# Kernel optimization log

Measured on AMD Instinct MI355X. Metric: run time of the kernel, lower is better.

Reference implementation:

```python
import jax, jax.numpy as jnp
import numpy as np

NUM_PT = 13
NUM_SQ = 64
SQPT = NUM_SQ * NUM_PT            # 832
NUM_FEATURES = NUM_SQ * SQPT      # 53248
ATTN_TABLE = NUM_SQ * SQPT * SQPT # 44302336
DEPTH = 256
DFF = 1024
NUM_HEADS = 4
N = 512
LN_EPS = 1e-5


def layer_norm(x, w, b):
    m = jnp.mean(x, axis=-1, keepdims=True)
    v = jnp.mean(jnp.square(x - m), axis=-1, keepdims=True)
    return (x - m) * jax.lax.rsqrt(v + LN_EPS) * w + b


def setup_inputs() -> dict:
    key = jax.random.key(0)
    ks = jax.random.split(key, 12)
    # indices must satisfy piece_indices = ksq*832 + offset, offset in [0,832)
    pno = jax.random.randint(ks[0], (N, NUM_SQ), 0, SQPT, dtype=jnp.int32)
    ksq = jax.random.randint(ks[1], (N,), 0, NUM_SQ, dtype=jnp.int32)
    piece_indices = ksq[:, None] * SQPT + pno
    attn_bias_indices = jax.random.randint(ks[2], (N, NUM_SQ * NUM_SQ), 0, NUM_PT * NUM_PT, dtype=jnp.int32)
    f32 = jnp.float32
    return {
        "piece_indices": piece_indices,
        "attn_bias_indices": attn_bias_indices,
        "ksq": ksq,
        "value_table": jax.random.normal(ks[3], (NUM_FEATURES, DEPTH), f32) * 0.02,
        "attn_weights_table": jax.random.normal(ks[4], (ATTN_TABLE, NUM_HEADS), f32) * 0.02,
        "attn_bias_table": jax.random.normal(ks[5], (NUM_PT * NUM_PT, NUM_HEADS), f32) * 0.02,
        "attn_scale": jnp.asarray(100.0, f32),
        "W1": jax.random.normal(ks[6], (DEPTH, DFF), f32) * 0.02,
        "b1": jnp.zeros((DFF,), f32),
        "W2": jax.random.normal(ks[7], (DFF, DEPTH), f32) * 0.02,
        "b2": jnp.zeros((DEPTH,), f32),
        "ln1_w": jnp.ones((DEPTH,), f32),
        "ln1_b": jnp.zeros((DEPTH,), f32),
        "ln2_w": jnp.ones((DEPTH,), f32),
        "ln2_b": jnp.zeros((DEPTH,), f32),
    }


def reference(piece_indices, attn_bias_indices, ksq, value_table, attn_weights_table,
              attn_bias_table, attn_scale, W1, b1, W2, b2, ln1_w, ln1_b, ln2_w, ln2_b):
    n = piece_indices.shape[0]
    dh = DEPTH // NUM_HEADS
    pno = piece_indices - ksq[:, None] * SQPT                      # [N,64] in [0,832)
    attn_idx = (pno[:, :, None] * SQPT + pno[:, None, :]
                + ksq[:, None, None] * SQPT * SQPT)                # [N,64,64]
    aw = attn_weights_table[attn_idx]                              # [N,64,64,H]
    abi = attn_bias_indices.reshape(n, NUM_SQ, NUM_SQ).transpose(0, 2, 1)
    ab = attn_bias_table[abi]                                      # [N,64,64,H]
    logits = ((aw + ab) * attn_scale).transpose(0, 3, 1, 2)        # [N,H,64,64]
    attn = jax.nn.softmax(logits, axis=-1)
    values = value_table[piece_indices].reshape(n, NUM_SQ, NUM_HEADS, dh).transpose(0, 2, 1, 3)  # [N,H,64,dh]
    ctx = jnp.einsum('nhqk,nhkd->nhqd', attn, values) + values
    x = layer_norm(ctx.transpose(0, 2, 1, 3).reshape(n, NUM_SQ, DEPTH), ln1_w, ln1_b)
    ffn = jnp.maximum(x @ W1 + b1, 0.0) @ W2 + b2
    return layer_norm(ffn + x, ln2_w, ln2_b)
```

## Files before the change

kernel.cpp:

```cpp
#include <hip/hip_runtime.h>
#include <stdint.h>

typedef unsigned short u16;
typedef __attribute__((ext_vector_type(8))) short bf16x8;
typedef __attribute__((ext_vector_type(4))) float f32x4;

typedef __attribute__((address_space(1))) const unsigned char gas_u8;
typedef __attribute__((address_space(3))) unsigned char las_u8;

__device__ __forceinline__ void gload_lds16(const void* g, void* l) {
  __builtin_amdgcn_global_load_lds((const gas_u8*)g, (las_u8*)l, 16, 0, 0);
}

__device__ __forceinline__ u16 f2bf(float f) {
  uint32_t u = __float_as_uint(f);
  u += 0x7fffu + ((u >> 16) & 1u);
  return (u16)(u >> 16);
}
__device__ __forceinline__ float bf2f(u16 v) {
  return __uint_as_float(((uint32_t)v) << 16);
}

__global__ __launch_bounds__(256, 4)
void transpose_kernel(const float* __restrict__ W1, u16* __restrict__ W1T,
                      const float* __restrict__ W2, u16* __restrict__ W2T) {
  __shared__ u16 tile[64 * 66];
  int b = blockIdx.x;
  const float* src; u16* dst; int R, C, tc, tr;
  if (b < 64) { src = W1; dst = W1T; R = 256; C = 1024; tc = (b & 15) * 64; tr = (b >> 4) * 64; }
  else { b -= 64; src = W2; dst = W2T; R = 1024; C = 256; tc = (b & 3) * 64; tr = (b >> 2) * 64; }
  const int t = threadIdx.x;
  const int c = t & 63, rb = t >> 6;
#pragma unroll
  for (int i = 0; i < 16; ++i) {
    int r = i * 4 + rb;
    tile[r * 66 + c] = f2bf(src[(size_t)(tr + r) * C + tc + c]);
  }
  __syncthreads();
#pragma unroll
  for (int i = 0; i < 16; ++i) {
    int x = i * 4 + rb;
    int y = c;
    dst[(size_t)(tc + x) * R + tr + y] = tile[y * 66 + x];
  }
}

#define SM_BASE 65536
#define OFF_ABT  (SM_BASE + 0)
#define OFF_PNO  (SM_BASE + 2704)
#define OFF_PIDX (SM_BASE + 2960)
#define OFF_REDA (SM_BASE + 3216)
#define OFF_REDB (SM_BASE + 7312)
#define OFF_RED  (SM_BASE + 11408)
#define OFF_HB   (SM_BASE + 0)

__global__ __launch_bounds__(256, 2)
void mega_kernel(const int* __restrict__ piece_indices,
                 const int* __restrict__ abi_idx,
                 const int* __restrict__ ksq,
                 const float* __restrict__ value_table,
                 const float* __restrict__ aw_table,
                 const float* __restrict__ ab_table,
                 const float* __restrict__ scale_p,
                 const float* __restrict__ ln1w, const float* __restrict__ ln1b,
                 const u16* __restrict__ W1T, const u16* __restrict__ W2T,
                 const float* __restrict__ b1, const float* __restrict__ b2,
                 const float* __restrict__ ln2w, const float* __restrict__ ln2b,
                 float* __restrict__ out) {
  __shared__ __align__(16) char SMEM[79872];
  u16* VT = (u16*)(SMEM);
  u16* P  = (u16*)(SMEM + 32768);
  float* abt_s = (float*)(SMEM + OFF_ABT);
  int* pno_s   = (int*)(SMEM + OFF_PNO);
  int* pidx_s  = (int*)(SMEM + OFF_PIDX);
  float* redA  = (float*)(SMEM + OFF_REDA);
  float* redB  = (float*)(SMEM + OFF_REDB);
  float* red   = (float*)(SMEM + OFF_RED);

  const int n = blockIdx.x;
  const int t = threadIdx.x;
  const int h = t >> 6;
  const int lane = t & 63;
  const int ks = ksq[n];

  if (t < 64) {
    int pi = piece_indices[n * 64 + t];
    pidx_s[t] = pi;
    pno_s[t] = pi - ks * 832;
  }
  for (int i = t; i < 676; i += 256) abt_s[i] = ab_table[i];
  __syncthreads();

  const float scale = scale_p[0];
  const int q = lane, kg = h;

  float l[4][16];
  {
    const int base = ks * (832 * 832) + pno_s[q] * 832;
#pragma unroll
    for (int j = 0; j < 16; ++j) {
      int k = kg * 16 + j;
      int idx = base + pno_s[k];
      f32x4 aw4 = *(const f32x4*)(aw_table + (size_t)idx * 4);
      int bi = abi_idx[n * 4096 + k * 64 + q];
      f32x4 ab4 = *(const f32x4*)(abt_s + bi * 4);
#pragma unroll
      for (int hh = 0; hh < 4; ++hh) l[hh][j] = (aw4[hh] + ab4[hh]) * scale;
    }
  }

  {
    const int feat = t;
#pragma unroll
    for (int c = 0; c < 8; ++c) {
      bf16x8 vv;
#pragma unroll
      for (int j = 0; j < 8; ++j) {
        int k = c * 8 + j;
        float v = value_table[(size_t)pidx_s[k] * 256 + feat];
        vv[j] = (short)f2bf(v);
      }
      int off = feat * 64 + ((c ^ (feat & 7)) << 3);
      *(bf16x8*)(&VT[off]) = vv;
    }
  }

#pragma unroll
  for (int hh = 0; hh < 4; ++hh) {
    float m = l[hh][0];
#pragma unroll
    for (int j = 1; j < 16; ++j) m = fmaxf(m, l[hh][j]);
    redA[(kg * 4 + hh) * 64 + q] = m;
  }
  __syncthreads();
  float inv[4];
#pragma unroll
  for (int hh = 0; hh < 4; ++hh) {
    float m = fmaxf(fmaxf(redA[(0 * 4 + hh) * 64 + q], redA[(1 * 4 + hh) * 64 + q]),
                    fmaxf(redA[(2 * 4 + hh) * 64 + q], redA[(3 * 4 + hh) * 64 + q]));
    float s = 0.f;
#pragma unroll
    for (int j = 0; j < 16; ++j) { l[hh][j] = __expf(l[hh][j] - m); s += l[hh][j]; }
    redB[(kg * 4 + hh) * 64 + q] = s;
  }
  __syncthreads();
#pragma unroll
  for (int hh = 0; hh < 4; ++hh)
    inv[hh] = 1.f / (redB[(0 * 4 + hh) * 64 + q] + redB[(1 * 4 + hh) * 64 + q] +
                     redB[(2 * 4 + hh) * 64 + q] + redB[(3 * 4 + hh) * 64 + q]);

#pragma unroll
  for (int hh = 0; hh < 4; ++hh) {
#pragma unroll
    for (int c2 = 0; c2 < 2; ++c2) {
      int c = kg * 2 + c2;
      bf16x8 pv;
#pragma unroll
      for (int j8 = 0; j8 < 8; ++j8) {
        int j = c2 * 8 + j8;
        int k = kg * 16 + j;
        float v = l[hh][j] * inv[hh] + ((k == q) ? 1.f : 0.f);
        pv[j8] = (short)f2bf(v);
      }
      int off = (hh * 64 + q) * 64 + ((c ^ (q & 7)) << 3);
      *(bf16x8*)(&P[off]) = pv;
    }
  }
  __syncthreads();

  const int li = lane & 15, lg = lane >> 4;
  f32x4 acc[4][4] = {};
#pragma unroll
  for (int kst = 0; kst < 2; ++kst) {
    int cg = kst * 4 + lg;
    bf16x8 aF[4], bF[4];
#pragma unroll
    for (int mi = 0; mi < 4; ++mi) {
      int row = mi * 16 + li;
      aF[mi] = *(const bf16x8*)(&P[(h * 64 + row) * 64 + ((cg ^ (row & 7)) << 3)]);
    }
#pragma unroll
    for (int ni = 0; ni < 4; ++ni) {
      int rr = h * 64 + ni * 16 + li;
      bF[ni] = *(const bf16x8*)(&VT[rr * 64 + ((cg ^ (rr & 7)) << 3)]);
    }
#pragma unroll
    for (int mi = 0; mi < 4; ++mi)
#pragma unroll
      for (int ni = 0; ni < 4; ++ni)
        acc[mi][ni] = __builtin_amdgcn_mfma_f32_16x16x32_bf16(aF[mi], bF[ni], acc[mi][ni], 0, 0, 0);
  }

#pragma unroll
  for (int mi = 0; mi < 4; ++mi)
#pragma unroll
    for (int r = 0; r < 4; ++r) {
      float s1 = 0.f, s2 = 0.f;
#pragma unroll
      for (int ni = 0; ni < 4; ++ni) { float v = acc[mi][ni][r]; s1 += v; s2 += v * v; }
#pragma unroll
      for (int mk = 1; mk < 16; mk <<= 1) { s1 += __shfl_xor(s1, mk, 64); s2 += __shfl_xor(s2, mk, 64); }
      if (li == 0) { int q2 = mi * 16 + lg * 4 + r; red[(h * 64 + q2) * 2 + 0] = s1; red[(h * 64 + q2) * 2 + 1] = s2; }
    }
  __syncthreads();

  u16* Xl = (u16*)(SMEM + 32768);
  {
    float w_[4], b_[4];
#pragma unroll
    for (int ni = 0; ni < 4; ++ni) {
      int f = h * 64 + ni * 16 + li;
      w_[ni] = ln1w[f]; b_[ni] = ln1b[f];
    }
#pragma unroll
    for (int mi = 0; mi < 4; ++mi)
#pragma unroll
      for (int r = 0; r < 4; ++r) {
        int q2 = mi * 16 + lg * 4 + r;
        float S1 = red[(0 * 64 + q2) * 2] + red[(1 * 64 + q2) * 2] +
                   red[(2 * 64 + q2) * 2] + red[(3 * 64 + q2) * 2];
        float S2 = red[(0 * 64 + q2) * 2 + 1] + red[(1 * 64 + q2) * 2 + 1] +
                   red[(2 * 64 + q2) * 2 + 1] + red[(3 * 64 + q2) * 2 + 1];
        float mean = S1 * (1.f / 256.f);
        float var = S2 * (1.f / 256.f) - mean * mean;
        float rs = rsqrtf(var + 1e-5f);
#pragma unroll
        for (int ni = 0; ni < 4; ++ni) {
          int col = h * 64 + ni * 16 + li;
          float xv = (acc[mi][ni][r] - mean) * rs * w_[ni] + b_[ni];
          int cc = col >> 3;
          *(u16*)((char*)Xl + q2 * 512 + (((cc ^ (q2 & 7)) & 31) << 4) + (col & 7) * 2) = f2bf(xv);
        }
      }
  }

  u16* Wb = (u16*)(SMEM);
  u16* Hb = (u16*)(SMEM + OFF_HB);
  const int wv = h;
  f32x4 oacc[4][4] = {};

  for (int ch = 0; ch < 16; ++ch) {
#pragma unroll
    for (int it = 0; it < 8; ++it) {
      int idx = it * 256 + t;
      int row = idx >> 5, c = idx & 31;
      const u16* g = W1T + (size_t)(ch * 64 + row) * 256 + (((c ^ (row & 7)) & 31) << 3);
      gload_lds16(g, (char*)Wb + it * 4096 + wv * 1024);
    }
    __syncthreads();

    f32x4 hacc[4] = {};
#pragma unroll
    for (int kst = 0; kst < 8; ++kst) {
      int cg = kst * 4 + lg;
      bf16x8 aF[4], bF;
      {
        int brow = wv * 16 + li;
        bF = *(const bf16x8*)((char*)Wb + brow * 512 + (((cg ^ (brow & 7)) & 31) << 4));
      }
#pragma unroll
      for (int mi = 0; mi < 4; ++mi) {
        int row = mi * 16 + li;
        aF[mi] = *(const bf16x8*)((char*)Xl + row * 512 + (((cg ^ (row & 7)) & 31) << 4));
      }
#pragma unroll
      for (int mi = 0; mi < 4; ++mi)
        hacc[mi] = __builtin_amdgcn_mfma_f32_16x16x32_bf16(aF[mi], bF, hacc[mi], 0, 0, 0);
    }
    __syncthreads();

    {
      float bv = b1[ch * 64 + wv * 16 + li];
      int col = wv * 16 + li;
      int c2 = col >> 3;
#pragma unroll
      for (int mi = 0; mi < 4; ++mi)
#pragma unroll
        for (int r = 0; r < 4; ++r) {
          int row = mi * 16 + lg * 4 + r;
          float v = fmaxf(hacc[mi][r] + bv, 0.f);
          *(u16*)((char*)Hb + row * 128 + ((c2 ^ (row & 7)) << 4) + (col & 7) * 2) = f2bf(v);
        }
    }
#pragma unroll
    for (int it = 0; it < 8; ++it) {
      int idx = it * 256 + t;
      int row = idx >> 3, c = idx & 7;
      const u16* g = W2T + (size_t)row * 1024 + ch * 64 + ((c ^ (row & 7)) << 3);
      gload_lds16(g, (char*)Wb + it * 4096 + wv * 1024);
    }
    __syncthreads();

#pragma unroll
    for (int kst = 0; kst < 2; ++kst) {
      int cg = kst * 4 + lg;
      bf16x8 aF[4], bF[4];
#pragma unroll
      for (int mi = 0; mi < 4; ++mi) {
        int row = mi * 16 + li;
        aF[mi] = *(const bf16x8*)((char*)Hb + row * 128 + (((cg ^ (row & 7)) & 7) << 4));
      }
#pragma unroll
      for (int ni = 0; ni < 4; ++ni) {
        int row = wv * 64 + ni * 16 + li;
        bF[ni] = *(const bf16x8*)((char*)Wb + row * 128 + (((cg ^ (row & 7)) & 7) << 4));
      }
#pragma unroll
      for (int mi = 0; mi < 4; ++mi)
#pragma unroll
        for (int ni = 0; ni < 4; ++ni)
          oacc[mi][ni] = __builtin_amdgcn_mfma_f32_16x16x32_bf16(aF[mi], bF[ni], oacc[mi][ni], 0, 0, 0);
    }
    __syncthreads();
  }

  float bias2[4];
#pragma unroll
  for (int ni = 0; ni < 4; ++ni) bias2[ni] = b2[wv * 64 + ni * 16 + li];

#pragma unroll
  for (int mi = 0; mi < 4; ++mi)
#pragma unroll
    for (int r = 0; r < 4; ++r) {
      float s1 = 0.f, s2 = 0.f;
      int row = mi * 16 + lg * 4 + r;
#pragma unroll
      for (int ni = 0; ni < 4; ++ni) {
        int col = wv * 64 + ni * 16 + li;
        int cc = col >> 3;
        u16 xres = *(const u16*)((char*)Xl + row * 512 + (((cc ^ (row & 7)) & 31) << 4) + (col & 7) * 2);
        float v = oacc[mi][ni][r] + bias2[ni] + bf2f(xres);
        oacc[mi][ni][r] = v;
        s1 += v; s2 += v * v;
      }
#pragma unroll
      for (int mk = 1; mk < 16; mk <<= 1) { s1 += __shfl_xor(s1, mk, 64); s2 += __shfl_xor(s2, mk, 64); }
      if (li == 0) { int q2 = mi * 16 + lg * 4 + r; red[(wv * 64 + q2) * 2 + 0] = s1; red[(wv * 64 + q2) * 2 + 1] = s2; }
    }
  __syncthreads();

  float lw[4], lb[4];
#pragma unroll
  for (int ni = 0; ni < 4; ++ni) {
    int col = wv * 64 + ni * 16 + li;
    lw[ni] = ln2w[col]; lb[ni] = ln2b[col];
  }
#pragma unroll
  for (int mi = 0; mi < 4; ++mi)
#pragma unroll
    for (int r = 0; r < 4; ++r) {
      int q2 = mi * 16 + lg * 4 + r;
      float S1 = red[(0 * 64 + q2) * 2] + red[(1 * 64 + q2) * 2] +
                 red[(2 * 64 + q2) * 2] + red[(3 * 64 + q2) * 2];
      float S2 = red[(0 * 64 + q2) * 2 + 1] + red[(1 * 64 + q2) * 2 + 1] +
                 red[(2 * 64 + q2) * 2 + 1] + red[(3 * 64 + q2) * 2 + 1];
      float mean = S1 * (1.f / 256.f);
      float var = S2 * (1.f / 256.f) - mean * mean;
      float rs = rsqrtf(var + 1e-5f);
      size_t rbase = (size_t)(n * 64 + q2) * 256;
#pragma unroll
      for (int ni = 0; ni < 4; ++ni)
        out[rbase + wv * 64 + ni * 16 + li] = (oacc[mi][ni][r] - mean) * rs * lw[ni] + lb[ni];
    }
}

extern "C" void kernel_launch(void* const* d_in, const int* in_sizes, int n_in,
                              void* d_out, int out_size, void* d_ws, size_t ws_size,
                              hipStream_t stream) {
  const int* piece_indices = (const int*)d_in[0];
  const int* abi_idx       = (const int*)d_in[1];
  const int* ksq           = (const int*)d_in[2];
  const float* value_table = (const float*)d_in[3];
  const float* aw_table    = (const float*)d_in[4];
  const float* ab_table    = (const float*)d_in[5];
  const float* attn_scale  = (const float*)d_in[6];
  const float* W1          = (const float*)d_in[7];
  const float* b1          = (const float*)d_in[8];
  const float* W2          = (const float*)d_in[9];
  const float* b2          = (const float*)d_in[10];
  const float* ln1w        = (const float*)d_in[11];
  const float* ln1b        = (const float*)d_in[12];
  const float* ln2w        = (const float*)d_in[13];
  const float* ln2b        = (const float*)d_in[14];

  char* ws = (char*)d_ws;
  u16* W1T = (u16*)(ws);
  u16* W2T = (u16*)(ws + (512 << 10));
  float* out = (float*)d_out;

  transpose_kernel<<<128, 256, 0, stream>>>(W1, W1T, W2, W2T);
  mega_kernel<<<512, 256, 0, stream>>>(piece_indices, abi_idx, ksq, value_table,
                                       aw_table, ab_table, attn_scale, ln1w, ln1b,
                                       W1T, W2T, b1, b2, ln2w, ln2b, out);
}
```

Measured before the change: 115.2 us.

## Coalesce attention-weight gathers via transposed load and LDS staging

Attention-weight rows are now loaded with lanes walking the contiguous key dimension (pno[q]*832 + pno[k] with the lane index on k), so adjacent lanes read nearby table entries. The values go through a swizzled shared-memory buffer, which is read back in the original query-major layout. Value-table loads are also issued early into registers and written to LDS later, so they overlap with the softmax work. The costs are an extra barrier, more shared memory use, and higher register pressure from holding the value fragments.

```diff
diff --git a/kernel.cpp b/kernel.cpp
--- a/kernel.cpp
+++ b/kernel.cpp
@@ -94,35 +94,48 @@
   const float scale = scale_p[0];
   const int q = lane, kg = h;
 
-  float l[4][16];
   {
-    const int base = ks * (832 * 832) + pno_s[q] * 832;
+    const int mypno = pno_s[lane];
+    const int base = ks * (832 * 832);
+    f32x4 awv[16];
 #pragma unroll
     for (int j = 0; j < 16; ++j) {
-      int k = kg * 16 + j;
-      int idx = base + pno_s[k];
-      f32x4 aw4 = *(const f32x4*)(aw_table + (size_t)idx * 4);
-      int bi = abi_idx[n * 4096 + k * 64 + q];
-      f32x4 ab4 = *(const f32x4*)(abt_s + bi * 4);
-#pragma unroll
-      for (int hh = 0; hh < 4; ++hh) l[hh][j] = (aw4[hh] + ab4[hh]) * scale;
-    }
-  }
-
+      int qj = h * 16 + j;
+      int idx = base + pno_s[qj] * 832 + mypno;
+      awv[j] = *(const f32x4*)(aw_table + (size_t)idx * 4);
+    }
+#pragma unroll
+    for (int j = 0; j < 16; ++j) {
+      int qj = h * 16 + j;
+      int slot = lane ^ qj;
+      *(f32x4*)(SMEM + qj * 1024 + (slot << 4)) = awv[j];
+    }
+  }
+  __syncthreads();
+
+  bf16x8 vreg[8];
   {
     const int feat = t;
 #pragma unroll
     for (int c = 0; c < 8; ++c) {
-      bf16x8 vv;
-#pragma unroll
-      for (int j = 0; j < 8; ++j) {
-        int k = c * 8 + j;
-        float v = value_table[(size_t)pidx_s[k] * 256 + feat];
-        vv[j] = (short)f2bf(v);
-      }
-      int off = feat * 64 + ((c ^ (feat & 7)) << 3);
-      *(bf16x8*)(&VT[off]) = vv;
-    }
+      float tmp[8];
+#pragma unroll
+      for (int jj = 0; jj < 8; ++jj)
+        tmp[jj] = value_table[(size_t)pidx_s[c * 8 + jj] * 256 + feat];
+#pragma unroll
+      for (int jj = 0; jj < 8; ++jj) vreg[c][jj] = (short)f2bf(tmp[jj]);
+    }
+  }
+
+  float l[4][16];
+#pragma unroll
+  for (int j = 0; j < 16; ++j) {
+    int k = kg * 16 + j;
+    f32x4 aw4 = *(const f32x4*)(SMEM + q * 1024 + ((k ^ q) << 4));
+    int bi = abi_idx[n * 4096 + k * 64 + q];
+    f32x4 ab4 = *(const f32x4*)(abt_s + bi * 4);
+#pragma unroll
+    for (int hh = 0; hh < 4; ++hh) l[hh][j] = (aw4[hh] + ab4[hh]) * scale;
   }
 
 #pragma unroll
@@ -164,6 +177,14 @@
       }
       int off = (hh * 64 + q) * 64 + ((c ^ (q & 7)) << 3);
       *(bf16x8*)(&P[off]) = pv;
+    }
+  }
+  {
+    const int feat = t;
+#pragma unroll
+    for (int c = 0; c < 8; ++c) {
+      int off = feat * 64 + ((c ^ (feat & 7)) << 3);
+      *(bf16x8*)(&VT[off]) = vreg[c];
     }
   }
   __syncthreads();
```

Measured after the change: 110.0 us. 1.05x faster.
